# Kernel optimization log

Hardware: AMD Instinct MI355X
Metric: run time of the kernel (lower is better)

Reference implementation:

```python
import jax, jax.numpy as jnp
import numpy as np

D_MODEL = 1024
NHEAD = 16
HEAD_DIM = D_MODEL // NHEAD
LN_EPS = 1e-5


def _layer_norm(x, g, b):
    mu = jnp.mean(x, axis=-1, keepdims=True)
    var = jnp.var(x, axis=-1, keepdims=True)
    return (x - mu) * jax.lax.rsqrt(var + LN_EPS) * g + b


def setup_inputs() -> dict:
    key = jax.random.key(0)
    ks = jax.random.split(key, 12)
    B, S = 2, 2048
    init = 0.02
    return {
        "query": jax.random.normal(ks[0], (B, S, D_MODEL), jnp.float32),
        "key_": jax.random.normal(ks[1], (B, S, D_MODEL), jnp.float32),
        "value": jax.random.normal(ks[2], (B, S, D_MODEL), jnp.float32),
        "Wq": jax.random.normal(ks[3], (D_MODEL, D_MODEL), jnp.float32) * init,
        "bq": jnp.zeros((D_MODEL,), jnp.float32),
        "Wk": jax.random.normal(ks[4], (D_MODEL, D_MODEL), jnp.float32) * init,
        "bk": jnp.zeros((D_MODEL,), jnp.float32),
        "Wv": jax.random.normal(ks[5], (D_MODEL, D_MODEL), jnp.float32) * init,
        "bv": jnp.zeros((D_MODEL,), jnp.float32),
        "Wo": jax.random.normal(ks[6], (D_MODEL, D_MODEL), jnp.float32) * init,
        "bo": jnp.zeros((D_MODEL,), jnp.float32),
        "ln_g": jnp.ones((D_MODEL,), jnp.float32),
        "ln_b": jnp.zeros((D_MODEL,), jnp.float32),
    }


def reference(query, key_, value, Wq, bq, Wk, bk, Wv, bv, Wo, bo, ln_g, ln_b):
    B, T, D = query.shape
    S = key_.shape[1]
    # shared LayerNorm applied to q, k, v inputs (as in the torch module)
    qn = _layer_norm(query, ln_g, ln_b)
    kn = _layer_norm(key_, ln_g, ln_b)
    vn = _layer_norm(value, ln_g, ln_b)
    # projections (torch Linear: x @ W.T + b)
    q = qn @ Wq.T + bq
    k = kn @ Wk.T + bk
    v = vn @ Wv.T + bv
    # [B, H, S, Dh]
    q = q.reshape(B, T, NHEAD, HEAD_DIM).transpose(0, 2, 1, 3)
    k = k.reshape(B, S, NHEAD, HEAD_DIM).transpose(0, 2, 1, 3)
    v = v.reshape(B, S, NHEAD, HEAD_DIM).transpose(0, 2, 1, 3)
    q = q * (HEAD_DIM ** -0.5)
    # [B, H, T, S] score matrix (explicitly materialized, as in source)
    scores = jnp.einsum("bhtd,bhsd->bhts", q, k)
    causal = jnp.triu(jnp.ones((T, S), dtype=bool), k=1)
    scores = jnp.where(causal, -jnp.inf, scores)
    attn = jax.nn.softmax(scores.astype(jnp.float32), axis=-1).astype(query.dtype)
    out = jnp.einsum("bhts,bhsd->bhtd", attn, v)
    out = out.transpose(0, 2, 1, 3).reshape(B, T, D)
    out = out @ Wo.T + bo
    return out, attn
```

## Files before the change

### kernel.cpp

```cpp
#include <hip/hip_runtime.h>
#include <hip/hip_bf16.h>

typedef unsigned short u16;
typedef __bf16 bf16x8 __attribute__((ext_vector_type(8)));
typedef float f32x4 __attribute__((ext_vector_type(4)));

__device__ __forceinline__ u16 f2bf(float f) {
  __hip_bfloat16 h = __float2bfloat16(f);
  u16 u;
  __builtin_memcpy(&u, &h, 2);
  return u;
}

__global__ __launch_bounds__(256) void ln_cast(
    const float* __restrict__ q, const float* __restrict__ k,
    const float* __restrict__ v, const float* __restrict__ g,
    const float* __restrict__ bb, u16* __restrict__ xn) {
  int row = blockIdx.x;
  int tsel = row >> 12;
  int r_in = row & 4095;
  const float* src = (tsel == 0) ? q : (tsel == 1) ? k : v;
  int tid = threadIdx.x;
  float4 x = ((const float4*)(src + (size_t)r_in * 1024))[tid];
  float s  = x.x + x.y + x.z + x.w;
  float ss = x.x * x.x + x.y * x.y + x.z * x.z + x.w * x.w;
  #pragma unroll
  for (int m = 1; m < 64; m <<= 1) { s += __shfl_xor(s, m); ss += __shfl_xor(ss, m); }
  __shared__ float red[8];
  int wid = tid >> 6;
  if ((tid & 63) == 0) { red[wid] = s; red[wid + 4] = ss; }
  __syncthreads();
  s  = red[0] + red[1] + red[2] + red[3];
  ss = red[4] + red[5] + red[6] + red[7];
  float mu  = s * (1.f / 1024.f);
  float var = ss * (1.f / 1024.f) - mu * mu;
  float rs  = rsqrtf(var + 1e-5f);
  float4 gv = ((const float4*)g)[tid];
  float4 bv = ((const float4*)bb)[tid];
  ushort4 o;
  o.x = f2bf((x.x - mu) * rs * gv.x + bv.x);
  o.y = f2bf((x.y - mu) * rs * gv.y + bv.y);
  o.z = f2bf((x.z - mu) * rs * gv.z + bv.z);
  o.w = f2bf((x.w - mu) * rs * gv.w + bv.w);
  ((ushort4*)(xn + (size_t)row * 1024))[tid] = o;
}

__global__ __launch_bounds__(256) void wcast(
    const float* __restrict__ wq, const float* __restrict__ wk,
    const float* __restrict__ wv, const float* __restrict__ wo,
    u16* __restrict__ dst) {
  int i = blockIdx.x * 256 + threadIdx.x;
  int e = i * 4;
  int sel = e >> 20;
  int loc = e & 1048575;
  const float* w = (sel == 0) ? wq : (sel == 1) ? wk : (sel == 2) ? wv : wo;
  float4 x = *(const float4*)(w + loc);
  ushort4 o;
  o.x = f2bf(x.x); o.y = f2bf(x.y); o.z = f2bf(x.z); o.w = f2bf(x.w);
  *(ushort4*)(dst + e) = o;
}

__global__ __launch_bounds__(256) void gemm_nt(
    const u16* __restrict__ A0, const u16* __restrict__ W0,
    const float* __restrict__ bias0, const float* __restrict__ bias1,
    const float* __restrict__ bias2,
    float* __restrict__ oF, u16* __restrict__ oP, int mode) {
  __shared__ alignas(16) u16 Al[128][40];
  __shared__ alignas(16) u16 Bl[128][40];
  int z = blockIdx.z;
  const u16* A = A0 + (size_t)z * 4194304;
  const u16* W = W0 + (size_t)z * 1048576;
  const float* bias = (z == 0) ? bias0 : (z == 1) ? bias1 : bias2;
  int m0 = blockIdx.y * 128, n0 = blockIdx.x * 128;
  int tid = threadIdx.x;
  int lane = tid & 63, wid = tid >> 6;
  int wr = wid >> 1, wc = wid & 1;
  int l15 = lane & 15, lg = lane >> 4;

  f32x4 acc[4][4];
  #pragma unroll
  for (int i = 0; i < 4; ++i)
    #pragma unroll
    for (int j = 0; j < 4; ++j) acc[i][j] = (f32x4){0.f, 0.f, 0.f, 0.f};

  for (int kt = 0; kt < 1024; kt += 32) {
    __syncthreads();
    #pragma unroll
    for (int c = tid; c < 512; c += 256) {
      int row = c >> 2, cb = c & 3;
      uint4 av = *(const uint4*)(A + (size_t)(m0 + row) * 1024 + kt + cb * 8);
      *(uint4*)&Al[row][cb * 8] = av;
      uint4 wv = *(const uint4*)(W + (size_t)(n0 + row) * 1024 + kt + cb * 8);
      *(uint4*)&Bl[row][cb * 8] = wv;
    }
    __syncthreads();
    bf16x8 af[4], bf[4];
    #pragma unroll
    for (int i = 0; i < 4; ++i)
      af[i] = *(const bf16x8*)&Al[wr * 64 + i * 16 + l15][lg * 8];
    #pragma unroll
    for (int j = 0; j < 4; ++j)
      bf[j] = *(const bf16x8*)&Bl[wc * 64 + j * 16 + l15][lg * 8];
    #pragma unroll
    for (int i = 0; i < 4; ++i)
      #pragma unroll
      for (int j = 0; j < 4; ++j)
        acc[i][j] = __builtin_amdgcn_mfma_f32_16x16x32_bf16(af[i], bf[j], acc[i][j], 0, 0, 0);
  }

  float scale = (mode == 1 && z == 0) ? 0.125f : 1.f;
  #pragma unroll
  for (int i = 0; i < 4; ++i) {
    #pragma unroll
    for (int j = 0; j < 4; ++j) {
      int n = n0 + wc * 64 + j * 16 + l15;
      float bn = bias[n];
      #pragma unroll
      for (int r = 0; r < 4; ++r) {
        int m = m0 + wr * 64 + i * 16 + lg * 4 + r;
        float val = (acc[i][j][r] + bn) * scale;
        if (mode == 0) {
          oF[(size_t)m * 1024 + n] = val;
        } else {
          int b = m >> 11, sIdx = m & 2047, h = n >> 6, d = n & 63;
          oP[(size_t)z * 4194304 +
             ((size_t)((b * 16 + h) * 2048 + sIdx)) * 64 + d] = f2bf(val);
        }
      }
    }
  }
}

__global__ __launch_bounds__(256) void attn_kernel(
    const u16* __restrict__ proj, float* __restrict__ attnOut,
    u16* __restrict__ oat) {
  __shared__ alignas(16) u16 Kl[64][72];
  __shared__ alignas(16) u16 Vt[64][72];
  __shared__ alignas(16) u16 Pl[4][16][72];
  const int t0 = blockIdx.x * 64;
  const int bh = blockIdx.y;
  const int tid = threadIdx.x;
  const int lane = tid & 63, w = tid >> 6;
  const int l15 = lane & 15, lg = lane >> 4;
  const u16* Q = proj;
  const u16* K = proj + 4194304;
  const u16* V = proj + 8388608;

  float* attnB = attnOut + ((size_t)bh * 2048) * 2048;

  {
    const int zc0 = t0 + 64;
    const int rowLen = (2048 - zc0) >> 2;
    const float4 z4 = make_float4(0.f, 0.f, 0.f, 0.f);
    for (int r = w; r < 64; r += 4) {
      float4* rp = (float4*)(attnB + (size_t)(t0 + r) * 2048 + zc0);
      for (int cc = lane; cc < rowLen; cc += 64) rp[cc] = z4;
    }
  }

  bf16x8 qa[2];
  {
    size_t qoff = ((size_t)bh * 2048 + t0 + w * 16 + l15) * 64 + lg * 8;
    qa[0] = *(const bf16x8*)(Q + qoff);
    qa[1] = *(const bf16x8*)(Q + qoff + 32);
  }
  const int jmax = t0 >> 6;

  float lsum[4] = {0.f, 0.f, 0.f, 0.f};
  for (int j = 0; j <= jmax; ++j) {
    __syncthreads();
    #pragma unroll
    for (int c = tid; c < 512; c += 256) {
      int row = c >> 3, cb = c & 7;
      uint4 kv = *(const uint4*)(K + ((size_t)bh * 2048 + j * 64 + row) * 64 + cb * 8);
      *(uint4*)&Kl[row][cb * 8] = kv;
    }
    __syncthreads();
    #pragma unroll
    for (int c = 0; c < 4; ++c) {
      f32x4 s = {0.f, 0.f, 0.f, 0.f};
      #pragma unroll
      for (int kb = 0; kb < 2; ++kb) {
        bf16x8 bfr = *(const bf16x8*)&Kl[c * 16 + l15][kb * 32 + lg * 8];
        s = __builtin_amdgcn_mfma_f32_16x16x32_bf16(qa[kb], bfr, s, 0, 0, 0);
      }
      int col = j * 64 + c * 16 + l15;
      #pragma unroll
      for (int r = 0; r < 4; ++r) {
        int trow = t0 + w * 16 + lg * 4 + r;
        if (col <= trow) lsum[r] += __expf(s[r]);
      }
    }
  }
  #pragma unroll
  for (int r = 0; r < 4; ++r) {
    #pragma unroll
    for (int m = 1; m < 16; m <<= 1) lsum[r] += __shfl_xor(lsum[r], m);
    lsum[r] = 1.f / lsum[r];
  }

  f32x4 acc_o[4];
  #pragma unroll
  for (int c2 = 0; c2 < 4; ++c2) acc_o[c2] = (f32x4){0.f, 0.f, 0.f, 0.f};

  for (int j = 0; j <= jmax; ++j) {
    __syncthreads();
    #pragma unroll
    for (int c = tid; c < 512; c += 256) {
      int row = c >> 3, cb = c & 7;
      size_t gof = ((size_t)bh * 2048 + j * 64 + row) * 64 + cb * 8;
      uint4 kv = *(const uint4*)(K + gof);
      *(uint4*)&Kl[row][cb * 8] = kv;
      uint4 vv = *(const uint4*)(V + gof);
      Vt[cb * 8 + 0][row] = (u16)(vv.x & 0xffff);
      Vt[cb * 8 + 1][row] = (u16)(vv.x >> 16);
      Vt[cb * 8 + 2][row] = (u16)(vv.y & 0xffff);
      Vt[cb * 8 + 3][row] = (u16)(vv.y >> 16);
      Vt[cb * 8 + 4][row] = (u16)(vv.z & 0xffff);
      Vt[cb * 8 + 5][row] = (u16)(vv.z >> 16);
      Vt[cb * 8 + 6][row] = (u16)(vv.w & 0xffff);
      Vt[cb * 8 + 7][row] = (u16)(vv.w >> 16);
    }
    __syncthreads();
    #pragma unroll
    for (int c = 0; c < 4; ++c) {
      f32x4 s = {0.f, 0.f, 0.f, 0.f};
      #pragma unroll
      for (int kb = 0; kb < 2; ++kb) {
        bf16x8 bfr = *(const bf16x8*)&Kl[c * 16 + l15][kb * 32 + lg * 8];
        s = __builtin_amdgcn_mfma_f32_16x16x32_bf16(qa[kb], bfr, s, 0, 0, 0);
      }
      int col = j * 64 + c * 16 + l15;
      #pragma unroll
      for (int r = 0; r < 4; ++r) {
        int trow = t0 + w * 16 + lg * 4 + r;
        float av = (col <= trow) ? __expf(s[r]) * lsum[r] : 0.f;
        attnB[(size_t)trow * 2048 + col] = av;
        Pl[w][lg * 4 + r][c * 16 + l15] = f2bf(av);
      }
    }
    __syncthreads();
    #pragma unroll
    for (int kb = 0; kb < 2; ++kb) {
      bf16x8 pa = *(const bf16x8*)&Pl[w][l15][kb * 32 + lg * 8];
      #pragma unroll
      for (int c2 = 0; c2 < 4; ++c2) {
        bf16x8 bv = *(const bf16x8*)&Vt[c2 * 16 + l15][kb * 32 + lg * 8];
        acc_o[c2] = __builtin_amdgcn_mfma_f32_16x16x32_bf16(pa, bv, acc_o[c2], 0, 0, 0);
      }
    }
  }

  int b = bh >> 4, h = bh & 15;
  #pragma unroll
  for (int c2 = 0; c2 < 4; ++c2) {
    #pragma unroll
    for (int r = 0; r < 4; ++r) {
      int trow = t0 + w * 16 + lg * 4 + r;
      oat[((size_t)(b * 2048 + trow)) * 1024 + h * 64 + c2 * 16 + l15] =
          f2bf(acc_o[c2][r]);
    }
  }
}

extern "C" void kernel_launch(void* const* d_in, const int* in_sizes, int n_in,
                              void* d_out, int out_size, void* d_ws, size_t ws_size,
                              hipStream_t stream) {
  const float* q    = (const float*)d_in[0];
  const float* k    = (const float*)d_in[1];
  const float* v    = (const float*)d_in[2];
  const float* Wq   = (const float*)d_in[3];
  const float* bq   = (const float*)d_in[4];
  const float* Wk   = (const float*)d_in[5];
  const float* bk   = (const float*)d_in[6];
  const float* Wv   = (const float*)d_in[7];
  const float* bv   = (const float*)d_in[8];
  const float* Wo   = (const float*)d_in[9];
  const float* bo   = (const float*)d_in[10];
  const float* ln_g = (const float*)d_in[11];
  const float* ln_b = (const float*)d_in[12];

  u16* ws   = (u16*)d_ws;
  u16* xn   = ws;
  u16* wb   = ws + 12582912;
  u16* proj = ws + 16777216;
  u16* oat  = ws + 29360128;
  float* out  = (float*)d_out;
  float* attn = out + 4194304;

  ln_cast<<<dim3(12288), dim3(256), 0, stream>>>(q, k, v, ln_g, ln_b, xn);
  wcast<<<dim3(4096), dim3(256), 0, stream>>>(Wq, Wk, Wv, Wo, wb);
  gemm_nt<<<dim3(8, 32, 3), dim3(256), 0, stream>>>(xn, wb, bq, bk, bv,
                                                    nullptr, proj, 1);
  attn_kernel<<<dim3(32, 32), dim3(256), 0, stream>>>(proj, attn, oat);
  gemm_nt<<<dim3(8, 32, 1), dim3(256), 0, stream>>>(oat, wb + 3 * 1048576, bo,
                                                    bo, bo, out, nullptr, 0);
}
```

Baseline: 828.4 us.

## Use direct global-to-LDS loads, pre-transposed V layout, and coalesced attention writes

The GEMM and attention kernels now use 16-byte global_load_lds transfers into unpadded LDS tiles, and the GEMM K-step grows from 32 to 64. The V projection is written by the GEMM epilogue directly in a transposed [bh][d][s] layout, which removes the scalar LDS transpose inside the attention loop. Attention probabilities are no longer stored from each lane as scattered fp32 values. They are read back from the bf16 LDS tile and written as coalesced float4 rows, meant to cut the cost of the large attn output. In exchange, the attn output now carries bf16-rounded values, and the unpadded LDS rows may cause bank conflicts on fragment reads.

Result: faster. 788.1 us (-4.9%).

```diff
diff --git a/kernel.cpp b/kernel.cpp
--- a/kernel.cpp
+++ b/kernel.cpp
@@ -2,6 +2,7 @@
 #include <hip/hip_bf16.h>
 
 typedef unsigned short u16;
+typedef unsigned int u32;
 typedef __bf16 bf16x8 __attribute__((ext_vector_type(8)));
 typedef float f32x4 __attribute__((ext_vector_type(4)));
 
@@ -10,6 +11,18 @@
   u16 u;
   __builtin_memcpy(&u, &h, 2);
   return u;
+}
+__device__ __forceinline__ float bf2f(u16 u) {
+  u32 b = ((u32)u) << 16;
+  float f;
+  __builtin_memcpy(&f, &b, 4);
+  return f;
+}
+
+__device__ __forceinline__ void gload16(const u16* g, u16* l) {
+  __builtin_amdgcn_global_load_lds(
+      (const __attribute__((address_space(1))) u32*)g,
+      (__attribute__((address_space(3))) u32*)l, 16, 0, 0);
 }
 
 __global__ __launch_bounds__(256) void ln_cast(
@@ -64,9 +77,10 @@
     const u16* __restrict__ A0, const u16* __restrict__ W0,
     const float* __restrict__ bias0, const float* __restrict__ bias1,
     const float* __restrict__ bias2,
-    float* __restrict__ oF, u16* __restrict__ oP, int mode) {
-  __shared__ alignas(16) u16 Al[128][40];
-  __shared__ alignas(16) u16 Bl[128][40];
+    float* __restrict__ oF, u16* __restrict__ oP, u16* __restrict__ oVT,
+    int mode) {
+  __shared__ alignas(16) u16 Al[128][64];
+  __shared__ alignas(16) u16 Bl[128][64];
   int z = blockIdx.z;
   const u16* A = A0 + (size_t)z * 4194304;
   const u16* W = W0 + (size_t)z * 1048576;
@@ -76,6 +90,7 @@
   int lane = tid & 63, wid = tid >> 6;
   int wr = wid >> 1, wc = wid & 1;
   int l15 = lane & 15, lg = lane >> 4;
+  int lr = lane >> 3, lc = lane & 7;
 
   f32x4 acc[4][4];
   #pragma unroll
@@ -83,29 +98,30 @@
     #pragma unroll
     for (int j = 0; j < 4; ++j) acc[i][j] = (f32x4){0.f, 0.f, 0.f, 0.f};
 
-  for (int kt = 0; kt < 1024; kt += 32) {
-    __syncthreads();
-    #pragma unroll
-    for (int c = tid; c < 512; c += 256) {
-      int row = c >> 2, cb = c & 3;
-      uint4 av = *(const uint4*)(A + (size_t)(m0 + row) * 1024 + kt + cb * 8);
-      *(uint4*)&Al[row][cb * 8] = av;
-      uint4 wv = *(const uint4*)(W + (size_t)(n0 + row) * 1024 + kt + cb * 8);
-      *(uint4*)&Bl[row][cb * 8] = wv;
-    }
-    __syncthreads();
-    bf16x8 af[4], bf[4];
-    #pragma unroll
-    for (int i = 0; i < 4; ++i)
-      af[i] = *(const bf16x8*)&Al[wr * 64 + i * 16 + l15][lg * 8];
-    #pragma unroll
-    for (int j = 0; j < 4; ++j)
-      bf[j] = *(const bf16x8*)&Bl[wc * 64 + j * 16 + l15][lg * 8];
-    #pragma unroll
-    for (int i = 0; i < 4; ++i)
+  for (int kt = 0; kt < 1024; kt += 64) {
+    __syncthreads();
+    #pragma unroll
+    for (int qq = 0; qq < 4; ++qq) {
+      int rb = (qq * 4 + wid) * 8;
+      gload16(A + (size_t)(m0 + rb + lr) * 1024 + kt + lc * 8, &Al[rb][0]);
+      gload16(W + (size_t)(n0 + rb + lr) * 1024 + kt + lc * 8, &Bl[rb][0]);
+    }
+    __syncthreads();
+    #pragma unroll
+    for (int kb = 0; kb < 2; ++kb) {
+      bf16x8 af[4], bw[4];
+      #pragma unroll
+      for (int i = 0; i < 4; ++i)
+        af[i] = *(const bf16x8*)&Al[wr * 64 + i * 16 + l15][kb * 32 + lg * 8];
       #pragma unroll
       for (int j = 0; j < 4; ++j)
-        acc[i][j] = __builtin_amdgcn_mfma_f32_16x16x32_bf16(af[i], bf[j], acc[i][j], 0, 0, 0);
+        bw[j] = *(const bf16x8*)&Bl[wc * 64 + j * 16 + l15][kb * 32 + lg * 8];
+      #pragma unroll
+      for (int i = 0; i < 4; ++i)
+        #pragma unroll
+        for (int j = 0; j < 4; ++j)
+          acc[i][j] = __builtin_amdgcn_mfma_f32_16x16x32_bf16(af[i], bw[j], acc[i][j], 0, 0, 0);
+    }
   }
 
   float scale = (mode == 1 && z == 0) ? 0.125f : 1.f;
@@ -123,8 +139,12 @@
           oF[(size_t)m * 1024 + n] = val;
         } else {
           int b = m >> 11, sIdx = m & 2047, h = n >> 6, d = n & 63;
-          oP[(size_t)z * 4194304 +
-             ((size_t)((b * 16 + h) * 2048 + sIdx)) * 64 + d] = f2bf(val);
+          if (z == 2) {
+            oVT[((size_t)((b * 16 + h) * 64 + d)) * 2048 + sIdx] = f2bf(val);
+          } else {
+            oP[(size_t)z * 4194304 +
+               ((size_t)((b * 16 + h) * 2048 + sIdx)) * 64 + d] = f2bf(val);
+          }
         }
       }
     }
@@ -132,19 +152,20 @@
 }
 
 __global__ __launch_bounds__(256) void attn_kernel(
-    const u16* __restrict__ proj, float* __restrict__ attnOut,
-    u16* __restrict__ oat) {
-  __shared__ alignas(16) u16 Kl[64][72];
-  __shared__ alignas(16) u16 Vt[64][72];
+    const u16* __restrict__ proj, const u16* __restrict__ vt,
+    float* __restrict__ attnOut, u16* __restrict__ oat) {
+  __shared__ alignas(16) u16 Kl[64][64];
+  __shared__ alignas(16) u16 Vt[64][64];
   __shared__ alignas(16) u16 Pl[4][16][72];
   const int t0 = blockIdx.x * 64;
   const int bh = blockIdx.y;
   const int tid = threadIdx.x;
   const int lane = tid & 63, w = tid >> 6;
   const int l15 = lane & 15, lg = lane >> 4;
+  const int lr = lane >> 3, lc = lane & 7;
   const u16* Q = proj;
   const u16* K = proj + 4194304;
-  const u16* V = proj + 8388608;
+  const u16* VT = vt + (size_t)bh * 131072;
 
   float* attnB = attnOut + ((size_t)bh * 2048) * 2048;
 
@@ -170,10 +191,9 @@
   for (int j = 0; j <= jmax; ++j) {
     __syncthreads();
     #pragma unroll
-    for (int c = tid; c < 512; c += 256) {
-      int row = c >> 3, cb = c & 7;
-      uint4 kv = *(const uint4*)(K + ((size_t)bh * 2048 + j * 64 + row) * 64 + cb * 8);
-      *(uint4*)&Kl[row][cb * 8] = kv;
+    for (int qq = 0; qq < 2; ++qq) {
+      int rb = (qq * 4 + w) * 8;
+      gload16(K + ((size_t)bh * 2048 + j * 64 + rb + lr) * 64 + lc * 8, &Kl[rb][0]);
     }
     __syncthreads();
     #pragma unroll
@@ -206,20 +226,10 @@
   for (int j = 0; j <= jmax; ++j) {
     __syncthreads();
     #pragma unroll
-    for (int c = tid; c < 512; c += 256) {
-      int row = c >> 3, cb = c & 7;
-      size_t gof = ((size_t)bh * 2048 + j * 64 + row) * 64 + cb * 8;
-      uint4 kv = *(const uint4*)(K + gof);
-      *(uint4*)&Kl[row][cb * 8] = kv;
-      uint4 vv = *(const uint4*)(V + gof);
-      Vt[cb * 8 + 0][row] = (u16)(vv.x & 0xffff);
-      Vt[cb * 8 + 1][row] = (u16)(vv.x >> 16);
-      Vt[cb * 8 + 2][row] = (u16)(vv.y & 0xffff);
-      Vt[cb * 8 + 3][row] = (u16)(vv.y >> 16);
-      Vt[cb * 8 + 4][row] = (u16)(vv.z & 0xffff);
-      Vt[cb * 8 + 5][row] = (u16)(vv.z >> 16);
-      Vt[cb * 8 + 6][row] = (u16)(vv.w & 0xffff);
-      Vt[cb * 8 + 7][row] = (u16)(vv.w >> 16);
+    for (int qq = 0; qq < 2; ++qq) {
+      int rb = (qq * 4 + w) * 8;
+      gload16(K + ((size_t)bh * 2048 + j * 64 + rb + lr) * 64 + lc * 8, &Kl[rb][0]);
+      gload16(VT + (size_t)(rb + lr) * 2048 + j * 64 + lc * 8, &Vt[rb][0]);
     }
     __syncthreads();
     #pragma unroll
@@ -235,11 +245,19 @@
       for (int r = 0; r < 4; ++r) {
         int trow = t0 + w * 16 + lg * 4 + r;
         float av = (col <= trow) ? __expf(s[r]) * lsum[r] : 0.f;
-        attnB[(size_t)trow * 2048 + col] = av;
         Pl[w][lg * 4 + r][c * 16 + l15] = f2bf(av);
       }
     }
     __syncthreads();
+    #pragma unroll
+    for (int rr = 0; rr < 4; ++rr) {
+      int flat = rr * 256 + tid;
+      int row = flat >> 4, c4 = flat & 15;
+      ushort4 p4 = *(const ushort4*)&Pl[row >> 4][row & 15][c4 * 4];
+      float4 f4;
+      f4.x = bf2f(p4.x); f4.y = bf2f(p4.y); f4.z = bf2f(p4.z); f4.w = bf2f(p4.w);
+      *(float4*)&attnB[(size_t)(t0 + row) * 2048 + j * 64 + c4 * 4] = f4;
+    }
     #pragma unroll
     for (int kb = 0; kb < 2; ++kb) {
       bf16x8 pa = *(const bf16x8*)&Pl[w][l15][kb * 32 + lg * 8];
@@ -284,6 +302,7 @@
   u16* xn   = ws;
   u16* wb   = ws + 12582912;
   u16* proj = ws + 16777216;
+  u16* vt   = ws + 25165824;
   u16* oat  = ws + 29360128;
   float* out  = (float*)d_out;
   float* attn = out + 4194304;
@@ -291,8 +310,8 @@
   ln_cast<<<dim3(12288), dim3(256), 0, stream>>>(q, k, v, ln_g, ln_b, xn);
   wcast<<<dim3(4096), dim3(256), 0, stream>>>(Wq, Wk, Wv, Wo, wb);
   gemm_nt<<<dim3(8, 32, 3), dim3(256), 0, stream>>>(xn, wb, bq, bk, bv,
-                                                    nullptr, proj, 1);
-  attn_kernel<<<dim3(32, 32), dim3(256), 0, stream>>>(proj, attn, oat);
+                                                    nullptr, proj, vt, 1);
+  attn_kernel<<<dim3(32, 32), dim3(256), 0, stream>>>(proj, vt, attn, oat);
   gemm_nt<<<dim3(8, 32, 1), dim3(256), 0, stream>>>(oat, wb + 3 * 1048576, bo,
-                                                    bo, bo, out, nullptr, 0);
-}
+                                                    bo, bo, out, nullptr, nullptr, 0);
+}
```
